# Performance work log

Measured on AMD Instinct MI355X. Metric: run time of the kernel, lower is better.

## Reference

```python
import jax, jax.numpy as jnp
import numpy as np
import math

B, N, EPG = 128, 512, 8192            # graphs, nodes/graph, edges/graph
E = B * EPG
DIN, H, DOUT = 128, 128, 10
RATIO = 0.8
K1 = math.ceil(RATIO * N)             # 410 nodes/graph after pool 1
K2 = math.ceil(RATIO * K1)            # 328 nodes/graph after pool 2
EPS = 1e-5


def setup_inputs() -> dict:
    key = jax.random.key(0)
    ks = jax.random.split(key, 16)
    x = jax.random.normal(ks[0], (B * N, DIN), jnp.float32)
    gid = jnp.repeat(jnp.arange(B, dtype=jnp.int32), EPG)
    src = jax.random.randint(ks[1], (E,), 0, N, dtype=jnp.int32) + gid * N
    dst = jax.random.randint(ks[2], (E,), 0, N, dtype=jnp.int32) + gid * N
    edge_index = jnp.stack([src, dst])

    def w(k, shape, fan_in):
        return jax.random.uniform(k, shape, jnp.float32, -1.0, 1.0) / np.sqrt(fan_in).astype(np.float32)

    return {
        "x": x, "edge_index": edge_index,
        "conv1_W": w(ks[3], (DIN, H), DIN), "conv1_b": jnp.zeros((H,), jnp.float32),
        "conv2_W": w(ks[4], (H, H), H),     "conv2_b": jnp.zeros((H,), jnp.float32),
        "score1_W": w(ks[5], (H, 1), H),    "score1_b": jnp.zeros((1,), jnp.float32),
        "score2_W": w(ks[6], (H, 1), H),    "score2_b": jnp.zeros((1,), jnp.float32),
        "bn1_g": jnp.ones((H,), jnp.float32), "bn1_b": jnp.zeros((H,), jnp.float32),
        "bn1_m": 0.1 * jax.random.normal(ks[7], (H,), jnp.float32),
        "bn1_v": jax.random.uniform(ks[8], (H,), jnp.float32, 0.5, 1.5),
        "bn2_g": jnp.ones((H,), jnp.float32), "bn2_b": jnp.zeros((H,), jnp.float32),
        "bn2_m": 0.1 * jax.random.normal(ks[9], (H,), jnp.float32),
        "bn2_v": jax.random.uniform(ks[10], (H,), jnp.float32, 0.5, 1.5),
        "lin0_W": w(ks[11], (DOUT, DIN), DIN), "lin0_b": jnp.zeros((DOUT,), jnp.float32),
        "lin1_W": w(ks[12], (DOUT, H), H),     "lin1_b": jnp.zeros((DOUT,), jnp.float32),
        "lin2_W": w(ks[13], (DOUT, H), H),     "lin2_b": jnp.zeros((DOUT,), jnp.float32),
    }


def gcn(h_in, src, dst, emask, W, b, n):
    # PyG GCNConv: self-loops + symmetric normalization D^-1/2 (A+I) D^-1/2 (XW) + b
    deg = jnp.ones((n,), h_in.dtype).at[dst].add(emask)      # self-loop counts as 1
    dinv = jax.lax.rsqrt(deg)
    coef = (dinv[src] * dinv[dst] * emask)[:, None]          # masked-out edges -> 0
    h = h_in @ W
    agg = jnp.zeros_like(h).at[dst].add(h[src] * coef)
    return agg + h * (dinv * dinv)[:, None] + b              # self-loop message + bias


def sag_pool(x, score, src, dst, emask, n_per, k):
    # topk per graph (equal-sized graphs -> static shapes), x <- x[perm]*tanh(score[perm])
    idx = jax.lax.top_k(score.reshape(B, n_per), k)[1]                      # [B,k]
    perm = (idx.astype(jnp.int32) + (jnp.arange(B, dtype=jnp.int32) * n_per)[:, None]).reshape(-1)
    xn = x[perm] * jnp.tanh(score[perm])[:, None]
    # filter_adj: remap surviving nodes, mask edges touching dropped nodes
    remap = jnp.full((B * n_per,), -1, jnp.int32).at[perm].set(jnp.arange(B * k, dtype=jnp.int32))
    s2, d2 = remap[src], remap[dst]
    em2 = emask * (s2 >= 0).astype(emask.dtype) * (d2 >= 0).astype(emask.dtype)
    return xn, jnp.maximum(s2, 0), jnp.maximum(d2, 0), em2


def bn_relu(x, g, b, m, v):
    # eval-mode BatchNorm1d followed by ReLU
    return jax.nn.relu(g * (x - m) * jax.lax.rsqrt(v + EPS) + b)


def reference(x, edge_index, conv1_W, conv1_b, conv2_W, conv2_b,
              score1_W, score1_b, score2_W, score2_b,
              bn1_g, bn1_b, bn1_m, bn1_v, bn2_g, bn2_b, bn2_m, bn2_v,
              lin0_W, lin0_b, lin1_W, lin1_b, lin2_W, lin2_b):
    src, dst = edge_index[0], edge_index[1]
    emask = jnp.ones((E,), x.dtype)
    hidden = [(x, N)]
    # layer 0: GCNConv -> SAGPool -> BN -> ReLU
    h = gcn(x, src, dst, emask, conv1_W, conv1_b, B * N)
    s = gcn(h, src, dst, emask, score1_W, score1_b, B * N)[:, 0]
    h, src, dst, emask = sag_pool(h, s, src, dst, emask, N, K1)
    h = bn_relu(h, bn1_g, bn1_b, bn1_m, bn1_v)
    hidden.append((h, K1))
    # layer 1
    h = gcn(h, src, dst, emask, conv2_W, conv2_b, B * K1)
    s = gcn(h, src, dst, emask, score2_W, score2_b, B * K1)[:, 0]
    h, src, dst, emask = sag_pool(h, s, src, dst, emask, K1, K2)
    h = bn_relu(h, bn2_g, bn2_b, bn2_m, bn2_v)
    hidden.append((h, K2))
    # jumping-knowledge readout: global_add_pool each rep, per-layer linear, sum (dropout eval = id)
    lins = [(lin0_W, lin0_b), (lin1_W, lin1_b), (lin2_W, lin2_b)]
    out = jnp.zeros((B, DOUT), x.dtype)
    for (hh, n_per), (W, bb) in zip(hidden, lins):
        pooled = hh.reshape(B, n_per, -1).sum(axis=1)   # global_add_pool (segment sum)
        out = out + pooled @ W.T + bb
    return out
```

## Files before the change

kernel.cpp:

```cpp
#include <hip/hip_runtime.h>

#define Bg   128
#define NPG  512
#define EPGc 8192
#define Etot (Bg*EPGc)
#define DOUTc 10
#define K1c  410
#define K2c  328
#define N0c  (Bg*NPG)
#define N1c  (Bg*K1c)
#define N2c  (Bg*K2c)
#define EPSc 1e-5f

static __global__ __launch_bounds__(512) void k_prep0(const int* __restrict__ src,
                                                      const int* __restrict__ dst,
                                                      float* __restrict__ dinv,
                                                      int* __restrict__ rp,
                                                      int2* __restrict__ e2,
                                                      float* __restrict__ pooled) {
  __shared__ int   cnt[NPG];
  __shared__ float sdv[NPG];
  __shared__ int   srp[NPG];
  __shared__ int   sbuf[512];
  int g = blockIdx.x, tid = threadIdx.x;
  if (tid < 128) {
    pooled[g * 128 + tid] = 0.f;
    pooled[Bg * 128 + g * 128 + tid] = 0.f;
    pooled[2 * Bg * 128 + g * 128 + tid] = 0.f;
  }
  cnt[tid] = 0;
  __syncthreads();
  const int* sp = src + (size_t)g * EPGc;
  const int* dp = dst + (size_t)g * EPGc;
  for (int e = tid; e < EPGc; e += 512) atomicAdd(&cnt[dp[e] - g * NPG], 1);
  __syncthreads();
  int c = cnt[tid];
  float dv = 1.0f / sqrtf(1.0f + (float)c);
  sdv[tid] = dv;
  dinv[g * NPG + tid] = dv;
  sbuf[tid] = c;
  __syncthreads();
  for (int off = 1; off < 512; off <<= 1) {
    int t = (tid >= off) ? sbuf[tid - off] : 0;
    __syncthreads();
    sbuf[tid] += t;
    __syncthreads();
  }
  srp[tid] = sbuf[tid] - c;
  rp[g * (NPG + 1) + tid] = sbuf[tid] - c;
  if (tid == 511) rp[g * (NPG + 1) + NPG] = sbuf[511];
  cnt[tid] = 0;
  __syncthreads();
  for (int e = tid; e < EPGc; e += 512) {
    int s = sp[e], d = dp[e];
    int dl = d - g * NPG;
    int pos = srp[dl] + atomicAdd(&cnt[dl], 1);
    e2[(size_t)g * EPGc + pos] =
        make_int2(s, __float_as_int(sdv[s - g * NPG] * sdv[dl]));
  }
}

static __global__ __launch_bounds__(512) void k_gemm2(const float* __restrict__ X,
                                                      const float* __restrict__ W,
                                                      float* __restrict__ Y, int M) {
  __shared__ float ws[128 * 128];
  __shared__ float xs[128 * 132];
  int tid = threadIdx.x;
  for (int i = tid; i < 4096; i += 512) ((float4*)ws)[i] = ((const float4*)W)[i];
  int row0 = blockIdx.x * 128;
  for (int i = tid; i < 4096; i += 512) {
    int r = i >> 5, kq = i & 31;
    float4 v = ((const float4*)X)[(size_t)(row0 + r) * 32 + kq];
    *(float4*)&xs[r * 132 + kq * 4] = v;
  }
  __syncthreads();
  int tx = tid & 15, ty = tid >> 4;
  float acc[4][8];
#pragma unroll
  for (int i = 0; i < 4; ++i)
#pragma unroll
    for (int j = 0; j < 8; ++j) acc[i][j] = 0.f;
  for (int k = 0; k < 128; k += 4) {
    float4 xr[4];
#pragma unroll
    for (int i = 0; i < 4; ++i) xr[i] = *(const float4*)&xs[(ty * 4 + i) * 132 + k];
    const float* xf = (const float*)xr;
#pragma unroll
    for (int kk = 0; kk < 4; ++kk) {
      float4 wa = *(const float4*)&ws[(k + kk) * 128 + tx * 4];
      float4 wb = *(const float4*)&ws[(k + kk) * 128 + 64 + tx * 4];
#pragma unroll
      for (int i = 0; i < 4; ++i) {
        float xv = xf[i * 4 + kk];
        acc[i][0] += xv * wa.x; acc[i][1] += xv * wa.y;
        acc[i][2] += xv * wa.z; acc[i][3] += xv * wa.w;
        acc[i][4] += xv * wb.x; acc[i][5] += xv * wb.y;
        acc[i][6] += xv * wb.z; acc[i][7] += xv * wb.w;
      }
    }
  }
#pragma unroll
  for (int i = 0; i < 4; ++i) {
    int row = row0 + ty * 4 + i;
    float4 o1 = make_float4(acc[i][0], acc[i][1], acc[i][2], acc[i][3]);
    float4 o2 = make_float4(acc[i][4], acc[i][5], acc[i][6], acc[i][7]);
    ((float4*)Y)[(size_t)row * 32 + tx] = o1;
    ((float4*)Y)[(size_t)row * 32 + 16 + tx] = o2;
  }
}

template <int NPER, int RG>
static __global__ __launch_bounds__(256) void k_agg3(const float* __restrict__ h0,
                                                     const float* __restrict__ dinv,
                                                     const float* __restrict__ bias,
                                                     const int* __restrict__ rp,
                                                     const int2* __restrict__ e2,
                                                     const float* __restrict__ sw,
                                                     float* __restrict__ h1,
                                                     float* __restrict__ spre) {
  int tid = threadIdx.x;
  int hw = tid >> 5, l = tid & 31;
  int b = blockIdx.x;
  int xcd = b & 7, slot = b >> 3;
  int g = xcd * 16 + (slot & 15);
  int rowgrp = slot >> 4;
  int li = rowgrp * 8 + hw;
  if (li >= NPER) return;
  int j = g * NPER + li;
  const int* rpg = rp + g * (NPER + 1);
  int start = rpg[li], end = rpg[li + 1];
  const int2* ep = e2 + (size_t)g * EPGc;
  float di = dinv[j];
  float sc = di * di;
  float4 acc = *(const float4*)&h0[(size_t)j * 128 + l * 4];
  float4 bb = ((const float4*)bias)[l];
  acc.x = acc.x * sc + bb.x; acc.y = acc.y * sc + bb.y;
  acc.z = acc.z * sc + bb.z; acc.w = acc.w * sc + bb.w;
  int e = start;
  for (; e + 4 <= end; e += 4) {
    int2 p0 = ep[e], p1 = ep[e + 1], p2 = ep[e + 2], p3 = ep[e + 3];
    float4 v0 = *(const float4*)&h0[(size_t)p0.x * 128 + l * 4];
    float4 v1 = *(const float4*)&h0[(size_t)p1.x * 128 + l * 4];
    float4 v2 = *(const float4*)&h0[(size_t)p2.x * 128 + l * 4];
    float4 v3 = *(const float4*)&h0[(size_t)p3.x * 128 + l * 4];
    float c0 = __int_as_float(p0.y), c1 = __int_as_float(p1.y);
    float c2 = __int_as_float(p2.y), c3 = __int_as_float(p3.y);
    acc.x += v0.x * c0 + v1.x * c1 + v2.x * c2 + v3.x * c3;
    acc.y += v0.y * c0 + v1.y * c1 + v2.y * c2 + v3.y * c3;
    acc.z += v0.z * c0 + v1.z * c1 + v2.z * c2 + v3.z * c3;
    acc.w += v0.w * c0 + v1.w * c1 + v2.w * c2 + v3.w * c3;
  }
  for (; e < end; ++e) {
    int2 pp = ep[e];
    float c = __int_as_float(pp.y);
    float4 v = *(const float4*)&h0[(size_t)pp.x * 128 + l * 4];
    acc.x += v.x * c; acc.y += v.y * c; acc.z += v.z * c; acc.w += v.w * c;
  }
  ((float4*)&h1[(size_t)j * 128])[l] = acc;
  float4 w4 = ((const float4*)sw)[l];
  float pr = acc.x * w4.x + acc.y * w4.y + acc.z * w4.z + acc.w * w4.w;
#pragma unroll
  for (int off = 16; off; off >>= 1) pr += __shfl_xor(pr, off, 64);
  if (l == 0) spre[j] = pr;
}

template <int NPER>
static __global__ void k_score2(const float* __restrict__ spre, const float* __restrict__ dinv,
                                const float* __restrict__ bptr, const int* __restrict__ rp,
                                const int2* __restrict__ e2, float* __restrict__ s, int n) {
  int j = blockIdx.x * 256 + threadIdx.x;
  if (j >= n) return;
  int g = j / NPER, li = j - g * NPER;
  const int* rpg = rp + g * (NPER + 1);
  int start = rpg[li], end = rpg[li + 1];
  const int2* ep = e2 + (size_t)g * EPGc;
  float di = dinv[j];
  float acc = spre[j] * di * di + bptr[0];
  int e = start;
  for (; e + 4 <= end; e += 4) {
    int2 p0 = ep[e], p1 = ep[e + 1], p2 = ep[e + 2], p3 = ep[e + 3];
    float a0 = spre[p0.x], a1 = spre[p1.x], a2 = spre[p2.x], a3 = spre[p3.x];
    acc += a0 * __int_as_float(p0.y) + a1 * __int_as_float(p1.y) +
           a2 * __int_as_float(p2.y) + a3 * __int_as_float(p3.y);
  }
  for (; e < end; ++e) { int2 pp = ep[e]; acc += spre[pp.x] * __int_as_float(pp.y); }
  s[j] = acc;
}

template <int NPER, int K>
static __global__ __launch_bounds__(512) void k_repool(const float* __restrict__ sv,
                                                       const int* __restrict__ src,
                                                       const int* __restrict__ dst,
                                                       int* __restrict__ perm,
                                                       float* __restrict__ dinv,
                                                       int* __restrict__ rp,
                                                       int2* __restrict__ e2) {
  __shared__ float sc[512];
  __shared__ int   sidx[512];
  __shared__ short remap[NPER];
  __shared__ int   cnt[K];
  __shared__ float sdv[K];
  __shared__ int   srp[K];
  __shared__ int   sbuf[512];
  int g = blockIdx.x, tid = threadIdx.x;
  sc[tid] = (tid < NPER) ? sv[g * NPER + tid] : -3.402823466e38f;
  sidx[tid] = tid;
  if (tid < NPER) remap[tid] = -1;
  __syncthreads();
  for (int kk = 2; kk <= 512; kk <<= 1) {
    for (int j = kk >> 1; j > 0; j >>= 1) {
      int i = tid, p = i ^ j;
      if (p > i) {
        bool up = ((i & kk) == 0);
        float si = sc[i], sp2 = sc[p];
        if (up ? (si < sp2) : (si > sp2)) {
          sc[i] = sp2; sc[p] = si;
          int t = sidx[i]; sidx[i] = sidx[p]; sidx[p] = t;
        }
      }
      __syncthreads();
    }
  }
  if (tid < K) {
    perm[g * K + tid] = g * NPER + sidx[tid];
    remap[sidx[tid]] = (short)tid;
    cnt[tid] = 0;
  }
  __syncthreads();
  const int* sp = src + (size_t)g * EPGc;
  const int* dp = dst + (size_t)g * EPGc;
  for (int e = tid; e < EPGc; e += 512) {
    int s = remap[sp[e] - g * NPER];
    int d = remap[dp[e] - g * NPER];
    if (s >= 0 && d >= 0) atomicAdd(&cnt[d], 1);
  }
  __syncthreads();
  int c = (tid < K) ? cnt[tid] : 0;
  if (tid < K) {
    float dv = 1.0f / sqrtf(1.0f + (float)c);
    sdv[tid] = dv;
    dinv[g * K + tid] = dv;
  }
  sbuf[tid] = c;
  __syncthreads();
  for (int off = 1; off < 512; off <<= 1) {
    int t = (tid >= off) ? sbuf[tid - off] : 0;
    __syncthreads();
    sbuf[tid] += t;
    __syncthreads();
  }
  if (tid < K) { srp[tid] = sbuf[tid] - c; rp[g * (K + 1) + tid] = sbuf[tid] - c; cnt[tid] = 0; }
  if (tid == 511) rp[g * (K + 1) + K] = sbuf[511];
  __syncthreads();
  for (int e = tid; e < EPGc; e += 512) {
    int s = remap[sp[e] - g * NPER];
    int d = remap[dp[e] - g * NPER];
    if (s >= 0 && d >= 0) {
      int pos = srp[d] + atomicAdd(&cnt[d], 1);
      e2[(size_t)g * EPGc + pos] = make_int2(g * K + s, __float_as_int(sdv[s] * sdv[d]));
    }
  }
}

template <int NPER, int K>
static __global__ __launch_bounds__(256) void k_topk(const float* __restrict__ s,
                                                     int* __restrict__ perm) {
  __shared__ float sc[512];
  __shared__ int   idx[512];
  int g = blockIdx.x, tid = threadIdx.x;
  for (int i = tid; i < 512; i += 256) {
    if (i < NPER) { sc[i] = s[g * NPER + i]; idx[i] = i; }
    else          { sc[i] = -3.402823466e38f; idx[i] = 0; }
  }
  __syncthreads();
  for (int kk = 2; kk <= 512; kk <<= 1) {
    for (int j = kk >> 1; j > 0; j >>= 1) {
      for (int base = 0; base < 512; base += 256) {
        int i = base + tid;
        int p = i ^ j;
        if (p > i) {
          bool up = ((i & kk) == 0);
          float si = sc[i], sp = sc[p];
          if (up ? (si < sp) : (si > sp)) {
            sc[i] = sp; sc[p] = si;
            int t = idx[i]; idx[i] = idx[p]; idx[p] = t;
          }
        }
      }
      __syncthreads();
    }
  }
  for (int r = tid; r < K; r += 256) perm[g * K + r] = g * NPER + idx[r];
}

template <int NPER, int CH>
static __global__ __launch_bounds__(128) void k_poolbn(const float* __restrict__ h,
                                                       const float* __restrict__ s,
                                                       const int* __restrict__ perm,
                                                       const float* __restrict__ gg,
                                                       const float* __restrict__ bb,
                                                       const float* __restrict__ mm,
                                                       const float* __restrict__ vv,
                                                       float* __restrict__ xp,
                                                       float* __restrict__ pooledseg) {
  int g = blockIdx.x / CH, cidx = blockIdx.x - g * CH;
  int f = threadIdx.x;
  const int rows = (NPER + CH - 1) / CH;
  int r0 = cidx * rows, r1 = min(NPER, r0 + rows);
  float G = gg[f], Bb = bb[f], Mm = mm[f];
  float inv = 1.0f / sqrtf(vv[f] + EPSc);
  float acc = 0.f;
  for (int r = r0; r < r1; ++r) {
    int j = g * NPER + r;
    int old = perm[j];
    float t = tanhf(s[old]);
    float val = h[(size_t)old * 128 + f] * t;
    float o = G * (val - Mm) * inv + Bb;
    o = fmaxf(o, 0.0f);
    xp[(size_t)j * 128 + f] = o;
    acc += o;
  }
  atomicAdd(&pooledseg[g * 128 + f], acc);
}

static __global__ __launch_bounds__(128) void k_gsum2(const float* __restrict__ xp,
                                                      float* __restrict__ pooled,
                                                      int nper, int nchunk) {
  int g = blockIdx.x / nchunk, c = blockIdx.x - g * nchunk;
  int f = threadIdx.x;
  int rows = (nper + nchunk - 1) / nchunk;
  int r0 = c * rows;
  int r1 = min(nper, r0 + rows);
  if (r0 >= r1) return;
  float acc = 0.f;
  const float* p = xp + ((size_t)g * nper + r0) * 128 + f;
  for (int i = r0; i < r1; ++i, p += 128) acc += *p;
  atomicAdd(&pooled[g * 128 + f], acc);
}

static __global__ void k_final(const float* __restrict__ pooled,
                               const float* __restrict__ w0, const float* __restrict__ b0,
                               const float* __restrict__ w1, const float* __restrict__ b1,
                               const float* __restrict__ w2, const float* __restrict__ b2,
                               float* __restrict__ out) {
  int t = blockIdx.x * 256 + threadIdx.x;
  if (t >= Bg * DOUTc) return;
  int g = t / DOUTc, o = t - g * DOUTc;
  const float* p0 = pooled + g * 128;
  const float* p1 = pooled + Bg * 128 + g * 128;
  const float* p2 = pooled + 2 * Bg * 128 + g * 128;
  float acc = b0[o] + b1[o] + b2[o];
  for (int k = 0; k < 128; ++k)
    acc += p0[k] * w0[o * 128 + k] + p1[k] * w1[o * 128 + k] + p2[k] * w2[o * 128 + k];
  out[t] = acc;
}

extern "C" void kernel_launch(void* const* d_in, const int* in_sizes, int n_in,
                              void* d_out, int out_size, void* d_ws, size_t ws_size,
                              hipStream_t stream) {
  (void)in_sizes; (void)n_in; (void)out_size; (void)ws_size;
  const float* x    = (const float*)d_in[0];
  const int*   ei   = (const int*)d_in[1];
  const int*   src0 = ei;
  const int*   dst0 = ei + Etot;
  const float* c1W = (const float*)d_in[2];  const float* c1b = (const float*)d_in[3];
  const float* c2W = (const float*)d_in[4];  const float* c2b = (const float*)d_in[5];
  const float* s1W = (const float*)d_in[6];  const float* s1b = (const float*)d_in[7];
  const float* s2W = (const float*)d_in[8];  const float* s2b = (const float*)d_in[9];
  const float* bn1g = (const float*)d_in[10]; const float* bn1b = (const float*)d_in[11];
  const float* bn1m = (const float*)d_in[12]; const float* bn1v = (const float*)d_in[13];
  const float* bn2g = (const float*)d_in[14]; const float* bn2b = (const float*)d_in[15];
  const float* bn2m = (const float*)d_in[16]; const float* bn2v = (const float*)d_in[17];
  const float* l0W = (const float*)d_in[18]; const float* l0b = (const float*)d_in[19];
  const float* l1W = (const float*)d_in[20]; const float* l1b = (const float*)d_in[21];
  const float* l2W = (const float*)d_in[22]; const float* l2b = (const float*)d_in[23];
  float* out = (float*)d_out;

  char* p = (char*)d_ws;
  auto alloc = [&](size_t bytes) { char* q = p; p += (bytes + 255) & ~(size_t)255; return q; };
  float* h0    = (float*)alloc((size_t)N0c * 128 * 4);
  float* h1    = (float*)alloc((size_t)N0c * 128 * 4);
  float* xp1   = (float*)alloc((size_t)N1c * 128 * 4);
  float* xp2   = (float*)alloc((size_t)N2c * 128 * 4);
  float* dinv  = (float*)alloc((size_t)N0c * 4);
  int*   rp    = (int*)alloc((size_t)Bg * (NPG + 1) * 4);
  int2*  e2    = (int2*)alloc((size_t)Etot * 8);
  float* spre  = (float*)alloc((size_t)N0c * 4);
  float* sv    = (float*)alloc((size_t)N0c * 4);
  int*   perm  = (int*)alloc((size_t)N1c * 4);
  float* pooled= (float*)alloc((size_t)3 * Bg * 128 * 4);

  dim3 b256(256), b128(128), b512(512);

  k_prep0<<<Bg, b512, 0, stream>>>(src0, dst0, dinv, rp, e2, pooled);
  k_gemm2<<<N0c / 128, b512, 0, stream>>>(x, c1W, h0, N0c);
  k_agg3<NPG, 64><<<128 * 64, b256, 0, stream>>>(h0, dinv, c1b, rp, e2, s1W, h1, spre);
  k_score2<NPG><<<(N0c + 255) / 256, b256, 0, stream>>>(spre, dinv, s1b, rp, e2, sv, N0c);
  k_repool<NPG, K1c><<<Bg, b512, 0, stream>>>(sv, src0, dst0, perm, dinv, rp, e2);
  k_poolbn<K1c, 8><<<Bg * 8, b128, 0, stream>>>(h1, sv, perm, bn1g, bn1b, bn1m, bn1v,
                                                xp1, pooled + Bg * 128);

  float* g1 = h0;
  float* h2 = h1;
  k_gemm2<<<N1c / 128, b512, 0, stream>>>(xp1, c2W, g1, N1c);
  k_agg3<K1c, 52><<<128 * 52, b256, 0, stream>>>(g1, dinv, c2b, rp, e2, s2W, h2, spre);
  k_score2<K1c><<<(N1c + 255) / 256, b256, 0, stream>>>(spre, dinv, s2b, rp, e2, sv, N1c);
  k_topk<K1c, K2c><<<Bg, b256, 0, stream>>>(sv, perm);
  k_poolbn<K2c, 8><<<Bg * 8, b128, 0, stream>>>(h2, sv, perm, bn2g, bn2b, bn2m, bn2v,
                                                xp2, pooled + 2 * Bg * 128);

  k_gsum2<<<Bg * 16, b128, 0, stream>>>(x, pooled, NPG, 16);
  k_final<<<(Bg * DOUTc + 255) / 256, b256, 0, stream>>>(pooled, l0W, l0b, l1W, l1b, l2W, l2b, out);
}
```

Baseline: 394.6 us.

## Use split-bf16 MFMA GEMM, fuse input readout into prep, skip dead pooled writes

Replaces the fp32 SIMT GEMM with an MFMA kernel that uses a three-term hi/lo bf16 split, approximating fp32 accuracy. The weights are pre-packed into the MFMA fragment layout by a new small kernel. The layer-0 global_add_pool is folded into the edge-prep kernel, which removes the separate gsum pass. The unused second-pool feature buffer write is dropped, and the aggregation loop gets an 8-way unrolled gather. Separate dinv/rowptr buffers are now used for the pooled graph. The split-bf16 scheme costs extra MFMA issues and carries a small precision risk.

```diff
diff --git a/kernel.cpp b/kernel.cpp
--- a/kernel.cpp
+++ b/kernel.cpp
@@ -12,24 +12,73 @@
 #define N2c  (Bg*K2c)
 #define EPSc 1e-5f
 
+typedef __attribute__((ext_vector_type(8))) short s8v;
+typedef __attribute__((ext_vector_type(4))) float f4v;
+
+static __device__ __forceinline__ unsigned short bf_rne(float x) {
+  unsigned u = __float_as_uint(x);
+  u += 0x7FFFu + ((u >> 16) & 1u);
+  return (unsigned short)(u >> 16);
+}
+static __device__ __forceinline__ float bf_f(unsigned short h) {
+  return __uint_as_float(((unsigned)h) << 16);
+}
+
+static __global__ void k_packW(const float* __restrict__ W1,
+                               const float* __restrict__ W2,
+                               unsigned short* __restrict__ pk) {
+  int i = blockIdx.x * 256 + threadIdx.x;
+  if (i >= 32768) return;
+  const float* W = (i < 16384) ? W1 : W2;
+  unsigned short* d = pk + ((i < 16384) ? 0 : 32768);
+  int ii = i & 16383;
+  int grp = ii >> 9, lane = (ii >> 3) & 63, j = ii & 7;
+  int kk = grp >> 3, t = grp & 7;
+  int k = kk * 32 + (lane >> 4) * 8 + j;
+  int n = t * 16 + (lane & 15);
+  float w = W[k * 128 + n];
+  unsigned short hi = bf_rne(w);
+  d[ii] = hi;
+  d[16384 + ii] = bf_rne(w - bf_f(hi));
+}
+
 static __global__ __launch_bounds__(512) void k_prep0(const int* __restrict__ src,
                                                       const int* __restrict__ dst,
+                                                      const float* __restrict__ x,
                                                       float* __restrict__ dinv,
                                                       int* __restrict__ rp,
                                                       int2* __restrict__ e2,
                                                       float* __restrict__ pooled) {
-  __shared__ int   cnt[NPG];
-  __shared__ float sdv[NPG];
-  __shared__ int   srp[NPG];
-  __shared__ int   sbuf[512];
+  __shared__ int    cnt[NPG];
+  __shared__ float  sdv[NPG];
+  __shared__ int    srp[NPG];
+  __shared__ int    sbuf[512];
+  __shared__ float4 xred[512];
   int g = blockIdx.x, tid = threadIdx.x;
+  cnt[tid] = 0;
   if (tid < 128) {
-    pooled[g * 128 + tid] = 0.f;
     pooled[Bg * 128 + g * 128 + tid] = 0.f;
     pooled[2 * Bg * 128 + g * 128 + tid] = 0.f;
   }
-  cnt[tid] = 0;
-  __syncthreads();
+  {
+    int c4 = tid & 31, rq = tid >> 5;
+    float4 a = make_float4(0.f, 0.f, 0.f, 0.f);
+    const float4* xp = (const float4*)(x + (size_t)g * NPG * 128);
+    for (int r = rq; r < NPG; r += 16) {
+      float4 v = xp[r * 32 + c4];
+      a.x += v.x; a.y += v.y; a.z += v.z; a.w += v.w;
+    }
+    xred[tid] = a;
+  }
+  __syncthreads();
+  if (tid < 32) {
+    float4 a = make_float4(0.f, 0.f, 0.f, 0.f);
+    for (int q = 0; q < 16; ++q) {
+      float4 v = xred[q * 32 + tid];
+      a.x += v.x; a.y += v.y; a.z += v.z; a.w += v.w;
+    }
+    ((float4*)&pooled[g * 128])[tid] = a;
+  }
   const int* sp = src + (size_t)g * EPGc;
   const int* dp = dst + (size_t)g * EPGc;
   for (int e = tid; e < EPGc; e += 512) atomicAdd(&cnt[dp[e] - g * NPG], 1);
@@ -60,52 +109,47 @@
   }
 }
 
-static __global__ __launch_bounds__(512) void k_gemm2(const float* __restrict__ X,
-                                                      const float* __restrict__ W,
-                                                      float* __restrict__ Y, int M) {
-  __shared__ float ws[128 * 128];
-  __shared__ float xs[128 * 132];
+static __global__ __launch_bounds__(256) void k_gemm3(const float* __restrict__ X,
+                                                      const unsigned short* __restrict__ pk,
+                                                      float* __restrict__ Y) {
+  __shared__ unsigned short wl[32768];
   int tid = threadIdx.x;
-  for (int i = tid; i < 4096; i += 512) ((float4*)ws)[i] = ((const float4*)W)[i];
-  int row0 = blockIdx.x * 128;
-  for (int i = tid; i < 4096; i += 512) {
-    int r = i >> 5, kq = i & 31;
-    float4 v = ((const float4*)X)[(size_t)(row0 + r) * 32 + kq];
-    *(float4*)&xs[r * 132 + kq * 4] = v;
-  }
-  __syncthreads();
-  int tx = tid & 15, ty = tid >> 4;
-  float acc[4][8];
-#pragma unroll
-  for (int i = 0; i < 4; ++i)
-#pragma unroll
-    for (int j = 0; j < 8; ++j) acc[i][j] = 0.f;
-  for (int k = 0; k < 128; k += 4) {
-    float4 xr[4];
-#pragma unroll
-    for (int i = 0; i < 4; ++i) xr[i] = *(const float4*)&xs[(ty * 4 + i) * 132 + k];
-    const float* xf = (const float*)xr;
+  for (int i = tid; i < 4096; i += 256) ((int4*)wl)[i] = ((const int4*)pk)[i];
+  int wv = tid >> 6, lane = tid & 63;
+  int q = lane >> 4, m16 = lane & 15;
+  size_t row = (size_t)blockIdx.x * 64 + wv * 16 + m16;
+  s8v ahi[4], alo[4];
+#pragma unroll
+  for (int kk = 0; kk < 4; ++kk) {
+    const float* xr = X + row * 128 + kk * 32 + q * 8;
+    float4 a0 = *(const float4*)xr;
+    float4 a1 = *(const float4*)(xr + 4);
+    float av[8] = {a0.x, a0.y, a0.z, a0.w, a1.x, a1.y, a1.z, a1.w};
+    union { unsigned short u[8]; s8v v; } H, L;
+#pragma unroll
+    for (int j = 0; j < 8; ++j) {
+      unsigned short h = bf_rne(av[j]);
+      H.u[j] = h;
+      L.u[j] = bf_rne(av[j] - bf_f(h));
+    }
+    ahi[kk] = H.v; alo[kk] = L.v;
+  }
+  __syncthreads();
+  int orow0 = blockIdx.x * 64 + wv * 16 + q * 4;
+#pragma unroll
+  for (int t = 0; t < 8; ++t) {
+    f4v acc = {0.f, 0.f, 0.f, 0.f};
 #pragma unroll
     for (int kk = 0; kk < 4; ++kk) {
-      float4 wa = *(const float4*)&ws[(k + kk) * 128 + tx * 4];
-      float4 wb = *(const float4*)&ws[(k + kk) * 128 + 64 + tx * 4];
-#pragma unroll
-      for (int i = 0; i < 4; ++i) {
-        float xv = xf[i * 4 + kk];
-        acc[i][0] += xv * wa.x; acc[i][1] += xv * wa.y;
-        acc[i][2] += xv * wa.z; acc[i][3] += xv * wa.w;
-        acc[i][4] += xv * wb.x; acc[i][5] += xv * wb.y;
-        acc[i][6] += xv * wb.z; acc[i][7] += xv * wb.w;
-      }
-    }
-  }
-#pragma unroll
-  for (int i = 0; i < 4; ++i) {
-    int row = row0 + ty * 4 + i;
-    float4 o1 = make_float4(acc[i][0], acc[i][1], acc[i][2], acc[i][3]);
-    float4 o2 = make_float4(acc[i][4], acc[i][5], acc[i][6], acc[i][7]);
-    ((float4*)Y)[(size_t)row * 32 + tx] = o1;
-    ((float4*)Y)[(size_t)row * 32 + 16 + tx] = o2;
+      s8v bhi = *(const s8v*)&wl[(kk * 8 + t) * 512 + lane * 8];
+      s8v blo = *(const s8v*)&wl[16384 + (kk * 8 + t) * 512 + lane * 8];
+      acc = __builtin_amdgcn_mfma_f32_16x16x32_bf16(ahi[kk], bhi, acc, 0, 0, 0);
+      acc = __builtin_amdgcn_mfma_f32_16x16x32_bf16(alo[kk], bhi, acc, 0, 0, 0);
+      acc = __builtin_amdgcn_mfma_f32_16x16x32_bf16(ahi[kk], blo, acc, 0, 0, 0);
+    }
+#pragma unroll
+    for (int r = 0; r < 4; ++r)
+      Y[(size_t)(orow0 + r) * 128 + t * 16 + m16] = acc[r];
   }
 }
 
@@ -137,6 +181,20 @@
   acc.x = acc.x * sc + bb.x; acc.y = acc.y * sc + bb.y;
   acc.z = acc.z * sc + bb.z; acc.w = acc.w * sc + bb.w;
   int e = start;
+  for (; e + 8 <= end; e += 8) {
+    int2 p[8];
+#pragma unroll
+    for (int qq = 0; qq < 8; ++qq) p[qq] = ep[e + qq];
+    float4 v[8];
+#pragma unroll
+    for (int qq = 0; qq < 8; ++qq) v[qq] = *(const float4*)&h0[(size_t)p[qq].x * 128 + l * 4];
+#pragma unroll
+    for (int qq = 0; qq < 8; ++qq) {
+      float c = __int_as_float(p[qq].y);
+      acc.x += v[qq].x * c; acc.y += v[qq].y * c;
+      acc.z += v[qq].z * c; acc.w += v[qq].w * c;
+    }
+  }
   for (; e + 4 <= end; e += 4) {
     int2 p0 = ep[e], p1 = ep[e + 1], p2 = ep[e + 2], p3 = ep[e + 3];
     float4 v0 = *(const float4*)&h0[(size_t)p0.x * 128 + l * 4];
@@ -192,12 +250,12 @@
                                                        const int* __restrict__ src,
                                                        const int* __restrict__ dst,
                                                        int* __restrict__ perm,
-                                                       float* __restrict__ dinv,
-                                                       int* __restrict__ rp,
+                                                       float* __restrict__ dinv2,
+                                                       int* __restrict__ rp2,
                                                        int2* __restrict__ e2) {
   __shared__ float sc[512];
   __shared__ int   sidx[512];
-  __shared__ short remap[NPER];
+  __shared__ short rmp[NPER];
   __shared__ int   cnt[K];
   __shared__ float sdv[K];
   __shared__ int   srp[K];
@@ -205,7 +263,7 @@
   int g = blockIdx.x, tid = threadIdx.x;
   sc[tid] = (tid < NPER) ? sv[g * NPER + tid] : -3.402823466e38f;
   sidx[tid] = tid;
-  if (tid < NPER) remap[tid] = -1;
+  if (tid < NPER) rmp[tid] = -1;
   __syncthreads();
   for (int kk = 2; kk <= 512; kk <<= 1) {
     for (int j = kk >> 1; j > 0; j >>= 1) {
@@ -223,23 +281,23 @@
   }
   if (tid < K) {
     perm[g * K + tid] = g * NPER + sidx[tid];
-    remap[sidx[tid]] = (short)tid;
+    rmp[sidx[tid]] = (short)tid;
     cnt[tid] = 0;
   }
   __syncthreads();
   const int* sp = src + (size_t)g * EPGc;
   const int* dp = dst + (size_t)g * EPGc;
   for (int e = tid; e < EPGc; e += 512) {
-    int s = remap[sp[e] - g * NPER];
-    int d = remap[dp[e] - g * NPER];
-    if (s >= 0 && d >= 0) atomicAdd(&cnt[d], 1);
+    int s = rmp[sp[e] - g * NPER];
+    int d = rmp[dp[e] - g * NPER];
+    if ((s | d) >= 0) atomicAdd(&cnt[d], 1);
   }
   __syncthreads();
   int c = (tid < K) ? cnt[tid] : 0;
   if (tid < K) {
     float dv = 1.0f / sqrtf(1.0f + (float)c);
     sdv[tid] = dv;
-    dinv[g * K + tid] = dv;
+    dinv2[g * K + tid] = dv;
   }
   sbuf[tid] = c;
   __syncthreads();
@@ -249,13 +307,13 @@
     sbuf[tid] += t;
     __syncthreads();
   }
-  if (tid < K) { srp[tid] = sbuf[tid] - c; rp[g * (K + 1) + tid] = sbuf[tid] - c; cnt[tid] = 0; }
-  if (tid == 511) rp[g * (K + 1) + K] = sbuf[511];
+  if (tid < K) { srp[tid] = sbuf[tid] - c; rp2[g * (K + 1) + tid] = sbuf[tid] - c; cnt[tid] = 0; }
+  if (tid == 511) rp2[g * (K + 1) + K] = sbuf[511];
   __syncthreads();
   for (int e = tid; e < EPGc; e += 512) {
-    int s = remap[sp[e] - g * NPER];
-    int d = remap[dp[e] - g * NPER];
-    if (s >= 0 && d >= 0) {
+    int s = rmp[sp[e] - g * NPER];
+    int d = rmp[dp[e] - g * NPER];
+    if ((s | d) >= 0) {
       int pos = srp[d] + atomicAdd(&cnt[d], 1);
       e2[(size_t)g * EPGc + pos] = make_int2(g * K + s, __float_as_int(sdv[s] * sdv[d]));
     }
@@ -293,7 +351,7 @@
   for (int r = tid; r < K; r += 256) perm[g * K + r] = g * NPER + idx[r];
 }
 
-template <int NPER, int CH>
+template <int NPER, int CH, bool WXP>
 static __global__ __launch_bounds__(128) void k_poolbn(const float* __restrict__ h,
                                                        const float* __restrict__ s,
                                                        const int* __restrict__ perm,
@@ -315,27 +373,11 @@
     int old = perm[j];
     float t = tanhf(s[old]);
     float val = h[(size_t)old * 128 + f] * t;
-    float o = G * (val - Mm) * inv + Bb;
-    o = fmaxf(o, 0.0f);
-    xp[(size_t)j * 128 + f] = o;
+    float o = fmaxf(G * (val - Mm) * inv + Bb, 0.f);
+    if (WXP) xp[(size_t)j * 128 + f] = o;
     acc += o;
   }
   atomicAdd(&pooledseg[g * 128 + f], acc);
-}
-
-static __global__ __launch_bounds__(128) void k_gsum2(const float* __restrict__ xp,
-                                                      float* __restrict__ pooled,
-                                                      int nper, int nchunk) {
-  int g = blockIdx.x / nchunk, c = blockIdx.x - g * nchunk;
-  int f = threadIdx.x;
-  int rows = (nper + nchunk - 1) / nchunk;
-  int r0 = c * rows;
-  int r1 = min(nper, r0 + rows);
-  if (r0 >= r1) return;
-  float acc = 0.f;
-  const float* p = xp + ((size_t)g * nper + r0) * 128 + f;
-  for (int i = r0; i < r1; ++i, p += 128) acc += *p;
-  atomicAdd(&pooled[g * 128 + f], acc);
 }
 
 static __global__ void k_final(const float* __restrict__ pooled,
@@ -381,34 +423,36 @@
   float* h0    = (float*)alloc((size_t)N0c * 128 * 4);
   float* h1    = (float*)alloc((size_t)N0c * 128 * 4);
   float* xp1   = (float*)alloc((size_t)N1c * 128 * 4);
-  float* xp2   = (float*)alloc((size_t)N2c * 128 * 4);
   float* dinv  = (float*)alloc((size_t)N0c * 4);
+  float* dinv2 = (float*)alloc((size_t)N1c * 4);
   int*   rp    = (int*)alloc((size_t)Bg * (NPG + 1) * 4);
+  int*   rp2   = (int*)alloc((size_t)Bg * (K1c + 1) * 4);
   int2*  e2    = (int2*)alloc((size_t)Etot * 8);
   float* spre  = (float*)alloc((size_t)N0c * 4);
   float* sv    = (float*)alloc((size_t)N0c * 4);
   int*   perm  = (int*)alloc((size_t)N1c * 4);
+  unsigned short* pk = (unsigned short*)alloc((size_t)65536 * 2);
   float* pooled= (float*)alloc((size_t)3 * Bg * 128 * 4);
 
-  dim3 b256(256), b128(128), b512(512);
-
-  k_prep0<<<Bg, b512, 0, stream>>>(src0, dst0, dinv, rp, e2, pooled);
-  k_gemm2<<<N0c / 128, b512, 0, stream>>>(x, c1W, h0, N0c);
+  dim3 b256(256), b512(512), b128(128);
+
+  k_packW<<<128, b256, 0, stream>>>(c1W, c2W, pk);
+  k_prep0<<<Bg, b512, 0, stream>>>(src0, dst0, x, dinv, rp, e2, pooled);
+  k_gemm3<<<N0c / 64, b256, 0, stream>>>(x, pk, h0);
   k_agg3<NPG, 64><<<128 * 64, b256, 0, stream>>>(h0, dinv, c1b, rp, e2, s1W, h1, spre);
   k_score2<NPG><<<(N0c + 255) / 256, b256, 0, stream>>>(spre, dinv, s1b, rp, e2, sv, N0c);
-  k_repool<NPG, K1c><<<Bg, b512, 0, stream>>>(sv, src0, dst0, perm, dinv, rp, e2);
-  k_poolbn<K1c, 8><<<Bg * 8, b128, 0, stream>>>(h1, sv, perm, bn1g, bn1b, bn1m, bn1v,
-                                                xp1, pooled + Bg * 128);
+  k_repool<NPG, K1c><<<Bg, b512, 0, stream>>>(sv, src0, dst0, perm, dinv2, rp2, e2);
+  k_poolbn<K1c, 8, true><<<Bg * 8, b128, 0, stream>>>(h1, sv, perm, bn1g, bn1b, bn1m, bn1v,
+                                                      xp1, pooled + Bg * 128);
 
   float* g1 = h0;
   float* h2 = h1;
-  k_gemm2<<<N1c / 128, b512, 0, stream>>>(xp1, c2W, g1, N1c);
-  k_agg3<K1c, 52><<<128 * 52, b256, 0, stream>>>(g1, dinv, c2b, rp, e2, s2W, h2, spre);
-  k_score2<K1c><<<(N1c + 255) / 256, b256, 0, stream>>>(spre, dinv, s2b, rp, e2, sv, N1c);
+  k_gemm3<<<N1c / 64, b256, 0, stream>>>(xp1, pk + 32768, g1);
+  k_agg3<K1c, 52><<<128 * 52, b256, 0, stream>>>(g1, dinv2, c2b, rp2, e2, s2W, h2, spre);
+  k_score2<K1c><<<(N1c + 255) / 256, b256, 0, stream>>>(spre, dinv2, s2b, rp2, e2, sv, N1c);
   k_topk<K1c, K2c><<<Bg, b256, 0, stream>>>(sv, perm);
-  k_poolbn<K2c, 8><<<Bg * 8, b128, 0, stream>>>(h2, sv, perm, bn2g, bn2b, bn2m, bn2v,
-                                                xp2, pooled + 2 * Bg * 128);
-
-  k_gsum2<<<Bg * 16, b128, 0, stream>>>(x, pooled, NPG, 16);
+  k_poolbn<K2c, 8, false><<<Bg * 8, b128, 0, stream>>>(h2, sv, perm, bn2g, bn2b, bn2m, bn2v,
+                                                       nullptr, pooled + 2 * Bg * 128);
+
   k_final<<<(Bg * DOUTc + 255) / 256, b256, 0, stream>>>(pooled, l0W, l0b, l1W, l1b, l2W, l2b, out);
 }
```

Result: faster. 385.1 us (-2.4%).
